# Optimization experiments

Measured on AMD Instinct MI355X. Metric: run time of the kernel, lower is better.

The kernel has to match this reference:

```python
import jax, jax.numpy as jnp
import numpy as np

B, C, H, W = 4, 64, 160, 160
O = 64
G = 4            # offset groups
KH = KW = 3
K = KH * KW
STRIDE, PAD = 1, 1


def setup_inputs() -> dict:
    key = jax.random.key(0)
    k1, k2, k3, k4, k5 = jax.random.split(key, 5)
    return {
        "warp_ref": jax.random.normal(k1, (B, C, H, W), jnp.float32),
        "offset_map": jax.random.normal(k2, (B, 2 * G * K, H, W), jnp.float32),
        "w_reg": jax.random.normal(k3, (O, C, KH, KW), jnp.float32) * 0.05,
        "w_mod": jax.random.normal(k4, (G * K, C, KH, KW), jnp.float32) * 0.05,
        "b_mod": jax.random.normal(k5, (G * K,), jnp.float32) * 0.05,
    }


def _conv2d(x, w, b):
    y = jax.lax.conv_general_dilated(x, w, (STRIDE, STRIDE), [(PAD, PAD), (PAD, PAD)],
                                     dimension_numbers=("NCHW", "OIHW", "NCHW"))
    return y + b[None, :, None, None]


def _deform_conv2d(x, offset, mask, weight):
    # Modulated deformable conv (DCNv2), torchvision semantics.
    b, c, h, w = x.shape
    ho, wo = h, w  # stride=1, pad=1, 3x3 -> same spatial size
    cg = c // G
    # offset layout: [B, 2*G*K, Ho, Wo] -> (group, kpos, (y, x))
    off = offset.reshape(b, G, K, 2, ho, wo)
    oy, ox = off[:, :, :, 0], off[:, :, :, 1]              # [B,G,K,Ho,Wo]
    ki, kj = jnp.meshgrid(jnp.arange(KH), jnp.arange(KW), indexing="ij")
    ki = ki.reshape(K).astype(x.dtype)
    kj = kj.reshape(K).astype(x.dtype)
    base_y = jnp.arange(ho, dtype=x.dtype) * STRIDE - PAD
    base_x = jnp.arange(wo, dtype=x.dtype) * STRIDE - PAD
    # absolute sampling positions [B,G,K,Ho,Wo]
    py = oy + base_y[None, None, None, :, None] + ki[None, None, :, None, None]
    px = ox + base_x[None, None, None, None, :] + kj[None, None, :, None, None]
    y0 = jnp.floor(py)
    x0 = jnp.floor(px)
    wy = py - y0
    wx = px - x0
    xg = x.reshape(b, G, cg, h * w)
    # gather per (batch, offset-group): xf [Cg, H*W], ix [K,Ho,Wo] -> [Cg,K,Ho,Wo]
    gather = jax.vmap(jax.vmap(lambda xf, ix: xf[:, ix]))

    def corner(yc, xc, cw):
        valid = (yc >= 0) & (yc < h) & (xc >= 0) & (xc < w)   # zero padding outside
        yi = jnp.clip(yc, 0, h - 1).astype(jnp.int32)
        xi = jnp.clip(xc, 0, w - 1).astype(jnp.int32)
        g = gather(xg, yi * w + xi)                            # [B,G,Cg,K,Ho,Wo]
        return g * (cw * valid.astype(x.dtype))[:, :, None]

    sampled = (corner(y0, x0, (1 - wy) * (1 - wx))
               + corner(y0, x0 + 1, (1 - wy) * wx)
               + corner(y0 + 1, x0, wy * (1 - wx))
               + corner(y0 + 1, x0 + 1, wy * wx))              # [B,G,Cg,K,Ho,Wo]
    wr = weight.reshape(weight.shape[0], G, cg, K)             # [O,G,Cg,K]
    m = mask.reshape(b, G, K, ho, wo)                          # modulation mask
    return jnp.einsum("ogck,bgckhw,bgkhw->bohw", wr, sampled, m)


def reference(warp_ref, offset_map, w_reg, w_mod, b_mod):
    h, w = warp_ref.shape[2], warp_ref.shape[3]
    offset_range = min(h, w) * 0.5 / 2
    off = offset_range * 2.0 * jax.nn.sigmoid(offset_map) - offset_range
    modulator = 2.0 * jax.nn.sigmoid(_conv2d(warp_ref, w_mod, b_mod))
    out = _deform_conv2d(warp_ref, off, modulator, w_reg)
    return out, off
```

## Files before the change

kernel.cpp:

```cpp
#include <hip/hip_runtime.h>

#define B_    4
#define C_    64
#define H_    160
#define W_    160
#define O_    64
#define G_    4
#define K_    9
#define CG_   16
#define MODC_ 36
#define OFFC_ 72
#define HW_   (H_*W_)

typedef __attribute__((ext_vector_type(8))) short short8;
typedef __attribute__((ext_vector_type(4))) float f32x4;
typedef __attribute__((ext_vector_type(2))) float f32x2;

#define NCHUNK_ 18

__device__ __forceinline__ float sigmoidf(float v) {
    return 1.0f / (1.0f + __expf(-v));
}

__device__ __forceinline__ short f2bf(float f) {
    unsigned u = __float_as_uint(f);
    u += 0x7FFFu + ((u >> 16) & 1u);
    return (short)(u >> 16);
}

__device__ __forceinline__ f32x2 unpk(unsigned u) {
    f32x2 r;
    r.x = __uint_as_float(u << 16);
    r.y = __uint_as_float(u & 0xffff0000u);
    return r;
}

__device__ __forceinline__ unsigned pack2(float a, float b) {
    unsigned ua = __float_as_uint(a) + 0x8000u;
    unsigned ub = __float_as_uint(b) + 0x8000u;
#if __has_builtin(__builtin_amdgcn_perm)
    return __builtin_amdgcn_perm(ub, ua, 0x07060302u);
#else
    return (ua >> 16) | (ub & 0xffff0000u);
#endif
}

__device__ __forceinline__ unsigned comb2(int a, int b, int c, int d,
                                          f32x2 w0, f32x2 w1, f32x2 w2, f32x2 w3) {
    f32x2 v = w0 * unpk((unsigned)a) + w1 * unpk((unsigned)b)
            + w2 * unpk((unsigned)c) + w3 * unpk((unsigned)d);
    return pack2(v.x, v.y);
}

__global__ __launch_bounds__(256) void k_prep(const float* __restrict__ x,
                                              const float* __restrict__ omap,
                                              const float* __restrict__ wreg,
                                              const float* __restrict__ wmod,
                                              unsigned short* __restrict__ xt,
                                              short* __restrict__ wA_def,
                                              short* __restrict__ wA_mod,
                                              float* __restrict__ out_off) {
    int blk = blockIdx.x;
    if (blk < 1600) {
        __shared__ unsigned short lds[256][17];
        int bg   = blk / 100;
        int pix0 = (blk % 100) * 256;
        const float* src = x + (size_t)bg * CG_ * HW_ + pix0;
#pragma unroll
        for (int c = 0; c < CG_; ++c)
            lds[threadIdx.x][c] = (unsigned short)f2bf(src[c * HW_ + threadIdx.x]);
        __syncthreads();
        unsigned w[8];
#pragma unroll
        for (int q = 0; q < 8; ++q)
            w[q] = (unsigned)lds[threadIdx.x][2 * q] |
                   ((unsigned)lds[threadIdx.x][2 * q + 1] << 16);
        uint4* dst = (uint4*)(xt + ((size_t)bg * HW_ + pix0 + threadIdx.x) * CG_);
        dst[0] = make_uint4(w[0], w[1], w[2], w[3]);
        dst[1] = make_uint4(w[4], w[5], w[6], w[7]);
    } else if (blk < 8800) {
        int i = (blk - 1600) * 256 + threadIdx.x;
        float4 v = ((const float4*)omap)[i];
        float4 r;
        r.x = 80.0f * sigmoidf(v.x) - 40.0f;
        r.y = 80.0f * sigmoidf(v.y) - 40.0f;
        r.z = 80.0f * sigmoidf(v.z) - 40.0f;
        r.w = 80.0f * sigmoidf(v.w) - 40.0f;
        ((float4*)out_off)[i] = r;
    } else {
        int tid = (blk - 8800) * 256 + threadIdx.x;
        if (tid < NCHUNK_ * 4 * 64) {
            int lane = tid & 63;
            int mt   = (tid >> 6) & 3;
            int cc   = tid >> 8;
            int quad = lane >> 4;
            int o    = mt * 16 + (lane & 15);
#pragma unroll
            for (int j = 0; j < 8; ++j) {
                int idx = cc * 32 + quad * 8 + j;
                int gk = idx >> 4, c = idx & 15;
                int g = gk / 9, kk = gk - g * 9;
                wA_def[(size_t)tid * 8 + j] = f2bf(wreg[((o * C_) + g * CG_ + c) * K_ + kk]);
            }
        } else {
            int t2 = tid - NCHUNK_ * 4 * 64;
            if (t2 < NCHUNK_ * 3 * 64) {
                int lane = t2 & 63;
                int mt   = (t2 >> 6) % 3;
                int cc   = t2 / 192;
                int quad = lane >> 4;
                int jch  = mt * 16 + (lane & 15);
#pragma unroll
                for (int j = 0; j < 8; ++j) {
                    int idx = cc * 32 + quad * 8 + j;
                    int t = idx >> 6, c = idx & 63;
                    float v = (jch < MODC_) ? wmod[((jch * C_) + c) * K_ + t] : 0.0f;
                    wA_mod[(size_t)t2 * 8 + j] = f2bf(v);
                }
            }
        }
    }
}


#define PREPB(cc_, par_) do {                                                  \
    int gk = (cc_) * 2 + qh;                                                   \
    int g  = gk / 9, kk = gk - g * 9;                                          \
    int ki = kk / 3, kj = kk - ki * 3;                                         \
    float fm = ml[gk * 16 + px];                                               \
    float py  = oy[cc_] + (float)(y - 1 + ki);                                 \
    float pxf = ox[cc_] + (float)(x - 1 + kj);                                 \
    float y0f = floorf(py), x0f = floorf(pxf);                                 \
    float wy = py - y0f, wx = pxf - x0f;                                       \
    int y0 = (int)y0f, x0i = (int)x0f;                                         \
    int y1 = y0 + 1, x1 = x0i + 1;                                             \
    float vy0 = ((unsigned)y0  < (unsigned)H_) ? 1.0f : 0.0f;                  \
    float vy1 = ((unsigned)y1  < (unsigned)H_) ? 1.0f : 0.0f;                  \
    float vx0 = ((unsigned)x0i < (unsigned)W_) ? 1.0f : 0.0f;                  \
    float vx1 = ((unsigned)x1  < (unsigned)W_) ? 1.0f : 0.0f;                  \
    int yc0 = min(max(y0, 0), H_ - 1);                                         \
    int yc1 = min(max(y1, 0), H_ - 1);                                         \
    int xc0 = min(max(x0i, 0), W_ - 1);                                        \
    int xc1 = min(max(x1, 0), W_ - 1);                                         \
    cw[par_][0] = (1.0f - wy) * (1.0f - wx) * vy0 * vx0 * fm;                  \
    cw[par_][1] = (1.0f - wy) * wx          * vy0 * vx1 * fm;                  \
    cw[par_][2] = wy * (1.0f - wx) * vy1 * vx0 * fm;                           \
    cw[par_][3] = wy * wx          * vy1 * vx1 * fm;                           \
    const unsigned short* xg = xt + ((size_t)(b * G_ + g) * HW_) * CG_ + cbase;\
    G[par_][0] = *(const int4*)(xg + (size_t)(yc0 * W_ + xc0) * CG_);          \
    G[par_][1] = *(const int4*)(xg + (size_t)(yc0 * W_ + xc1) * CG_);          \
    G[par_][2] = *(const int4*)(xg + (size_t)(yc1 * W_ + xc0) * CG_);          \
    G[par_][3] = *(const int4*)(xg + (size_t)(yc1 * W_ + xc1) * CG_);          \
} while (0)

#define CONSB(cc_, par_) do {                                                  \
    f32x2 w0 = {cw[par_][0], cw[par_][0]};                                     \
    f32x2 w1 = {cw[par_][1], cw[par_][1]};                                     \
    f32x2 w2 = {cw[par_][2], cw[par_][2]};                                     \
    f32x2 w3 = {cw[par_][3], cw[par_][3]};                                     \
    int4 bi;                                                                   \
    bi.x = (int)comb2(G[par_][0].x, G[par_][1].x, G[par_][2].x, G[par_][3].x,  \
                      w0, w1, w2, w3);                                         \
    bi.y = (int)comb2(G[par_][0].y, G[par_][1].y, G[par_][2].y, G[par_][3].y,  \
                      w0, w1, w2, w3);                                         \
    bi.z = (int)comb2(G[par_][0].z, G[par_][1].z, G[par_][2].z, G[par_][3].z,  \
                      w0, w1, w2, w3);                                         \
    bi.w = (int)comb2(G[par_][0].w, G[par_][1].w, G[par_][2].w, G[par_][3].w,  \
                      w0, w1, w2, w3);                                         \
    short8 bfr = *(short8*)&bi;                                                \
    const short8* wp = wa + (cc_) * 256;                                       \
    acc0 = __builtin_amdgcn_mfma_f32_16x16x32_bf16(wp[lane],       bfr, acc0, 0, 0, 0); \
    acc1 = __builtin_amdgcn_mfma_f32_16x16x32_bf16(wp[64 + lane],  bfr, acc1, 0, 0, 0); \
    acc2 = __builtin_amdgcn_mfma_f32_16x16x32_bf16(wp[128 + lane], bfr, acc2, 0, 0, 0); \
    acc3 = __builtin_amdgcn_mfma_f32_16x16x32_bf16(wp[192 + lane], bfr, acc3, 0, 0, 0); \
} while (0)

__global__ __launch_bounds__(256, 4) void k_fused(const unsigned short* __restrict__ xt,
                                                  const float* __restrict__ out_off,
                                                  const short* __restrict__ wA_mod,
                                                  const short* __restrict__ wA_def,
                                                  const float* __restrict__ bm,
                                                  float* __restrict__ out) {
    __shared__ float modl[4][MODC_][16];
    int b    = (blockIdx.x & 7) >> 1;
    int tile = ((blockIdx.x >> 3) << 1) + (blockIdx.x & 1);
    int wave = threadIdx.x >> 6;
    int lane = threadIdx.x & 63;
    int quad = lane >> 4;
    int px   = lane & 15;
    int p    = tile * 64 + wave * 16 + px;
    int y    = p / W_;
    int x    = p - y * W_;

    f32x4 m0 = {}, m1 = {}, m2 = {};
    const short8* wm = (const short8*)wA_mod;

#pragma unroll
    for (int cc = 0; cc < NCHUNK_; ++cc) {
        int t  = cc >> 1;
        int dy = t / 3 - 1;
        int dx = t - (t / 3) * 3 - 1;
        int yy = y + dy, xx = x + dx;
        bool ok = (((unsigned)yy < (unsigned)H_) && ((unsigned)xx < (unsigned)W_));
        int yc = min(max(yy, 0), H_ - 1);
        int xc = min(max(xx, 0), W_ - 1);
        int ch0 = (cc & 1) * 32 + (quad << 3);
        int g   = ch0 >> 4;
        int cl  = ch0 & 15;
        int4 raw = *(const int4*)(xt + ((size_t)(b * G_ + g) * HW_ +
                                        (size_t)(yc * W_ + xc)) * CG_ + cl);
        if (!ok) raw = make_int4(0, 0, 0, 0);
        short8 bfr = *(short8*)&raw;

        const short8* w = wm + cc * 192;
        m0 = __builtin_amdgcn_mfma_f32_16x16x32_bf16(w[lane],       bfr, m0, 0, 0, 0);
        m1 = __builtin_amdgcn_mfma_f32_16x16x32_bf16(w[64 + lane],  bfr, m1, 0, 0, 0);
        m2 = __builtin_amdgcn_mfma_f32_16x16x32_bf16(w[128 + lane], bfr, m2, 0, 0, 0);
    }

    float* ml = &modl[wave][0][0];
#pragma unroll
    for (int reg = 0; reg < 4; ++reg) {
        int j0 = quad * 4 + reg;
        ml[j0 * 16 + px]        = 2.0f * sigmoidf(m0[reg] + bm[j0]);
        ml[(16 + j0) * 16 + px] = 2.0f * sigmoidf(m1[reg] + bm[16 + j0]);
        if (32 + j0 < MODC_)
            ml[(32 + j0) * 16 + px] = 2.0f * sigmoidf(m2[reg] + bm[32 + j0]);
    }

    f32x4 acc0 = {}, acc1 = {}, acc2 = {}, acc3 = {};
    const float* offp = out_off + (size_t)b * OFFC_ * HW_ + p;
    const short8* wa  = (const short8*)wA_def;
    int qh    = quad >> 1;
    int cbase = (quad & 1) * 8;

    float oy[NCHUNK_], ox[NCHUNK_];
#pragma unroll
    for (int cc = 0; cc < NCHUNK_; ++cc) {
        int gk = cc * 2 + qh;
        int g  = gk / 9, kk = gk - g * 9;
        oy[cc] = offp[(size_t)(g * 18 + kk * 2) * HW_];
        ox[cc] = offp[(size_t)(g * 18 + kk * 2 + 1) * HW_];
    }

    int4  G[2][4];
    float cw[2][4];

    PREPB(0, 0);
#pragma unroll
    for (int cc = 0; cc < NCHUNK_ - 1; ++cc) {
        PREPB(cc + 1, (cc + 1) & 1);
        CONSB(cc, cc & 1);
    }
    CONSB(NCHUNK_ - 1, (NCHUNK_ - 1) & 1);

    float* op = out + (size_t)b * O_ * HW_ + p;
#pragma unroll
    for (int reg = 0; reg < 4; ++reg) {
        int o0 = quad * 4 + reg;
        op[(size_t)o0 * HW_]        = acc0[reg];
        op[(size_t)(16 + o0) * HW_] = acc1[reg];
        op[(size_t)(32 + o0) * HW_] = acc2[reg];
        op[(size_t)(48 + o0) * HW_] = acc3[reg];
    }
}

extern "C" void kernel_launch(void* const* d_in, const int* in_sizes, int n_in,
                              void* d_out, int out_size, void* d_ws, size_t ws_size,
                              hipStream_t stream) {
    const float* warp = (const float*)d_in[0];
    const float* omap = (const float*)d_in[1];
    const float* wreg = (const float*)d_in[2];
    const float* wmod = (const float*)d_in[3];
    const float* bmod = (const float*)d_in[4];

    float* out     = (float*)d_out;
    float* out_off = out + (size_t)B_ * O_ * HW_;

    unsigned short* xt = (unsigned short*)d_ws;
    short* wA_def = (short*)(xt + (size_t)B_ * C_ * HW_);
    short* wA_mod = wA_def + NCHUNK_ * 4 * 64 * 8;

    hipLaunchKernelGGL(k_prep, dim3(8832), dim3(256), 0, stream,
                       warp, omap, wreg, wmod, xt, wA_def, wA_mod, out_off);
    hipLaunchKernelGGL(k_fused, dim3(1600), dim3(256), 0, stream,
                       xt, out_off, wA_mod, wA_def, bmod, out);
}
```

Baseline: 189.2 us.

## Fuse offset sigmoid into main kernel and shrink blocks to one wave

```diff
diff --git a/kernel.cpp b/kernel.cpp
--- a/kernel.cpp
+++ b/kernel.cpp
@@ -53,13 +53,11 @@
 }
 
 __global__ __launch_bounds__(256) void k_prep(const float* __restrict__ x,
-                                              const float* __restrict__ omap,
                                               const float* __restrict__ wreg,
                                               const float* __restrict__ wmod,
                                               unsigned short* __restrict__ xt,
                                               short* __restrict__ wA_def,
-                                              short* __restrict__ wA_mod,
-                                              float* __restrict__ out_off) {
+                                              short* __restrict__ wA_mod) {
     int blk = blockIdx.x;
     if (blk < 1600) {
         __shared__ unsigned short lds[256][17];
@@ -78,17 +76,8 @@
         uint4* dst = (uint4*)(xt + ((size_t)bg * HW_ + pix0 + threadIdx.x) * CG_);
         dst[0] = make_uint4(w[0], w[1], w[2], w[3]);
         dst[1] = make_uint4(w[4], w[5], w[6], w[7]);
-    } else if (blk < 8800) {
-        int i = (blk - 1600) * 256 + threadIdx.x;
-        float4 v = ((const float4*)omap)[i];
-        float4 r;
-        r.x = 80.0f * sigmoidf(v.x) - 40.0f;
-        r.y = 80.0f * sigmoidf(v.y) - 40.0f;
-        r.z = 80.0f * sigmoidf(v.z) - 40.0f;
-        r.w = 80.0f * sigmoidf(v.w) - 40.0f;
-        ((float4*)out_off)[i] = r;
     } else {
-        int tid = (blk - 8800) * 256 + threadIdx.x;
+        int tid = (blk - 1600) * 256 + threadIdx.x;
         if (tid < NCHUNK_ * 4 * 64) {
             int lane = tid & 63;
             int mt   = (tid >> 6) & 3;
@@ -175,20 +164,21 @@
     acc3 = __builtin_amdgcn_mfma_f32_16x16x32_bf16(wp[192 + lane], bfr, acc3, 0, 0, 0); \
 } while (0)
 
-__global__ __launch_bounds__(256, 4) void k_fused(const unsigned short* __restrict__ xt,
-                                                  const float* __restrict__ out_off,
-                                                  const short* __restrict__ wA_mod,
-                                                  const short* __restrict__ wA_def,
-                                                  const float* __restrict__ bm,
-                                                  float* __restrict__ out) {
-    __shared__ float modl[4][MODC_][16];
-    int b    = (blockIdx.x & 7) >> 1;
-    int tile = ((blockIdx.x >> 3) << 1) + (blockIdx.x & 1);
-    int wave = threadIdx.x >> 6;
-    int lane = threadIdx.x & 63;
+__global__ __launch_bounds__(64) void k_fused(const unsigned short* __restrict__ xt,
+                                              const float* __restrict__ omap,
+                                              const short* __restrict__ wA_mod,
+                                              const short* __restrict__ wA_def,
+                                              const float* __restrict__ bm,
+                                              float* __restrict__ out,
+                                              float* __restrict__ out_off) {
+    __shared__ float modl[MODC_][16];
+    int blk  = blockIdx.x;
+    int b    = (blk & 7) >> 1;
+    int tile = ((blk >> 3) << 1) + (blk & 1);
+    int lane = threadIdx.x;
     int quad = lane >> 4;
     int px   = lane & 15;
-    int p    = tile * 64 + wave * 16 + px;
+    int p    = tile * 16 + px;
     int y    = p / W_;
     int x    = p - y * W_;
 
@@ -218,7 +208,7 @@
         m2 = __builtin_amdgcn_mfma_f32_16x16x32_bf16(w[128 + lane], bfr, m2, 0, 0, 0);
     }
 
-    float* ml = &modl[wave][0][0];
+    float* ml = &modl[0][0];
 #pragma unroll
     for (int reg = 0; reg < 4; ++reg) {
         int j0 = quad * 4 + reg;
@@ -229,7 +219,8 @@
     }
 
     f32x4 acc0 = {}, acc1 = {}, acc2 = {}, acc3 = {};
-    const float* offp = out_off + (size_t)b * OFFC_ * HW_ + p;
+    const float* omp  = omap + (size_t)b * OFFC_ * HW_ + p;
+    float*       offw = out_off + (size_t)b * OFFC_ * HW_ + p;
     const short8* wa  = (const short8*)wA_def;
     int qh    = quad >> 1;
     int cbase = (quad & 1) * 8;
@@ -239,8 +230,14 @@
     for (int cc = 0; cc < NCHUNK_; ++cc) {
         int gk = cc * 2 + qh;
         int g  = gk / 9, kk = gk - g * 9;
-        oy[cc] = offp[(size_t)(g * 18 + kk * 2) * HW_];
-        ox[cc] = offp[(size_t)(g * 18 + kk * 2 + 1) * HW_];
+        float ry = omp[(size_t)(g * 18 + kk * 2) * HW_];
+        float rx = omp[(size_t)(g * 18 + kk * 2 + 1) * HW_];
+        oy[cc] = 80.0f * sigmoidf(ry) - 40.0f;
+        ox[cc] = 80.0f * sigmoidf(rx) - 40.0f;
+        if ((quad & 1) == 0) {
+            offw[(size_t)(g * 18 + kk * 2) * HW_]     = oy[cc];
+            offw[(size_t)(g * 18 + kk * 2 + 1) * HW_] = ox[cc];
+        }
     }
 
     int4  G[2][4];
@@ -281,8 +278,8 @@
     short* wA_def = (short*)(xt + (size_t)B_ * C_ * HW_);
     short* wA_mod = wA_def + NCHUNK_ * 4 * 64 * 8;
 
-    hipLaunchKernelGGL(k_prep, dim3(8832), dim3(256), 0, stream,
-                       warp, omap, wreg, wmod, xt, wA_def, wA_mod, out_off);
-    hipLaunchKernelGGL(k_fused, dim3(1600), dim3(256), 0, stream,
-                       xt, out_off, wA_mod, wA_def, bmod, out);
-}
+    hipLaunchKernelGGL(k_prep, dim3(1632), dim3(256), 0, stream,
+                       warp, wreg, wmod, xt, wA_def, wA_mod);
+    hipLaunchKernelGGL(k_fused, dim3(6400), dim3(64), 0, stream,
+                       xt, omap, wA_mod, wA_def, bmod, out, out_off);
+}
```

Result: slower. 212.9 us (+12.5%).
